# Performance work log

Hardware: AMD Instinct MI355X
Metric: run time of the kernel (lower is better)

Reference implementation:

```python
import jax, jax.numpy as jnp
import numpy as np

N = 100000   # nodes
E = 1600000  # edges
D = 64       # in_feats
H = 512      # hidden_dim
O = 64       # out_feats
K = 3        # hops
LN_EPS = 1e-5


def setup_inputs() -> dict:
    key = jax.random.key(0)
    ks = jax.random.split(key, 10)
    x = jax.random.normal(ks[0], (N, D), dtype=jnp.float32)
    edge_index = jax.random.randint(ks[1], (2, E), 0, N, dtype=jnp.int64)
    # SAGEConv lin_l weights (root_weight=False, bias=False): K stacked [D, D]
    w_prop = jax.random.normal(ks[2], (K, D, D), dtype=jnp.float32) / np.sqrt(D)
    lin1_w = jax.random.normal(ks[3], ((K + 1) * D, H), dtype=jnp.float32) / np.sqrt((K + 1) * D)
    lin1_b = jnp.zeros((H,), dtype=jnp.float32)
    ln_gamma = jnp.ones((H,), dtype=jnp.float32)
    ln_beta = jnp.zeros((H,), dtype=jnp.float32)
    lin2_w = jax.random.normal(ks[4], (H, O), dtype=jnp.float32) / np.sqrt(H)
    lin2_b = jnp.zeros((O,), dtype=jnp.float32)
    return {
        "x": x, "edge_index": edge_index, "w_prop": w_prop,
        "lin1_w": lin1_w, "lin1_b": lin1_b,
        "ln_gamma": ln_gamma, "ln_beta": ln_beta,
        "lin2_w": lin2_w, "lin2_b": lin2_b,
    }


def _sage_mean(h, src, dst, w):
    # mean-aggregate neighbor features at dst, then linear (no root, no bias)
    msg_sum = jax.ops.segment_sum(h[src], dst, num_segments=N)       # [N, D]
    deg = jax.ops.segment_sum(jnp.ones((E,), h.dtype), dst, num_segments=N)
    agg = msg_sum / jnp.maximum(deg, 1.0)[:, None]
    return agg @ w


def reference(x, edge_index, w_prop, lin1_w, lin1_b, ln_gamma, ln_beta, lin2_w, lin2_b):
    src, dst = edge_index[0], edge_index[1]
    zs = [x]
    curr = x
    for i in range(K):
        curr = _sage_mean(curr, src, dst, w_prop[i])
        zs.append(curr)
    h = jnp.concatenate(zs, axis=1)          # [N, (K+1)*D]
    h = h @ lin1_w + lin1_b                   # [N, H]
    mu = jnp.mean(h, axis=-1, keepdims=True)
    var = jnp.var(h, axis=-1, keepdims=True)
    h = (h - mu) * jax.lax.rsqrt(var + LN_EPS) * ln_gamma + ln_beta
    h = jax.nn.relu(h)
    # dropout is identity in eval mode (training=False)
    return h @ lin2_w + lin2_b                # [N, O]
```

## Files before the change

kernel.cpp:

```cpp
#include <hip/hip_runtime.h>

constexpr int NN = 100000;
constexpr int NE = 1600000;
constexpr int NBUK = 196;
constexpr int ECAP = 10240;
constexpr int CHUNK = 6250;
constexpr int NPT = 13;

typedef __attribute__((ext_vector_type(8))) short bf16x8;
typedef __attribute__((ext_vector_type(4))) float f32x4;

__device__ inline ushort f2b(float f){
  uint u = __float_as_uint(f);
  uint r = (u + 0x7FFFu + ((u >> 16) & 1u)) >> 16;
  return (ushort)r;
}
__device__ inline float b2f(ushort u){
  uint v = ((uint)u) << 16;
  return __uint_as_float(v);
}

template<int CTRL>
__device__ inline float dpp_xadd(float v){
  int j = __builtin_amdgcn_update_dpp(0, __float_as_int(v), CTRL, 0xF, 0xF, true);
  return v + __int_as_float(j);
}
__device__ inline float red16(float v){
  v = dpp_xadd<0xB1>(v);
  v = dpp_xadd<0x4E>(v);
  v = dpp_xadd<0x141>(v);
  v = dpp_xadd<0x140>(v);
  return v;
}

__global__ __launch_bounds__(512) void k_part1(const int* __restrict__ srcA,
                                               const int* __restrict__ dstA,
                                               int* __restrict__ bukcur,
                                               int* __restrict__ ebuf){
  __shared__ int stage[CHUNK];
  __shared__ unsigned char bstage[CHUNK];
  __shared__ int hist[256];
  __shared__ int lofs[256];
  __shared__ int lcur[NBUK];
  __shared__ int basebuf[NBUK];
  int t = threadIdx.x;
  int cbase = blockIdx.x * CHUNK;

  if (t < 256) hist[t] = 0;
  if (t < NBUK) lcur[t] = 0;
  __syncthreads();

  int pk[NPT], bb[NPT];
  #pragma unroll
  for (int j = 0; j < NPT; ++j){
    int i = t + j*512;
    bb[j] = -1;
    if (i < CHUNK){
      int e = cbase + i;
      int d = dstA[e];
      bb[j] = d >> 9;
      pk[j] = (srcA[e] << 9) | (d & 511);
      atomicAdd(&hist[bb[j]], 1);
    }
  }
  __syncthreads();

  int v = (t < 256) ? hist[t] : 0;
  if (t < 256) lofs[t] = v;
  __syncthreads();
  #pragma unroll
  for (int off = 1; off < 256; off <<= 1){
    int tv = (t < 256 && t >= off) ? lofs[t-off] : 0;
    __syncthreads();
    if (t < 256) lofs[t] += tv;
    __syncthreads();
  }
  if (t < 256) lofs[t] -= v;
  if (t < NBUK) basebuf[t] = atomicAdd(&bukcur[t], v);
  __syncthreads();

  #pragma unroll
  for (int j = 0; j < NPT; ++j){
    if (bb[j] >= 0){
      int p = atomicAdd(&lcur[bb[j]], 1);
      int slot = lofs[bb[j]] + p;
      stage[slot] = pk[j];
      bstage[slot] = (unsigned char)bb[j];
    }
  }
  __syncthreads();

  for (int i = t; i < CHUNK; i += 512){
    int b = bstage[i];
    int j = i - lofs[b];
    int pos = basebuf[b] + j;
    if (pos < ECAP) ebuf[b*ECAP + pos] = stage[i];
  }
}

__global__ void k_bscan(const int* __restrict__ bukcur, int* __restrict__ bukptr){
  __shared__ int s[256];
  int t = threadIdx.x;
  int v = (t < NBUK) ? bukcur[t] : 0;
  s[t] = v; __syncthreads();
  #pragma unroll
  for (int off = 1; off < 256; off <<= 1){
    int tv = (t >= off) ? s[t-off] : 0;
    __syncthreads();
    s[t] += tv;
    __syncthreads();
  }
  if (t < NBUK) bukptr[t] = s[t] - v;
  if (t == NBUK-1) bukptr[NBUK] = s[t];
}

__global__ __launch_bounds__(512) void k_bfinal(const int* __restrict__ ebuf,
                                                const int* __restrict__ bukcur,
                                                const int* __restrict__ bukptr,
                                                int* __restrict__ rowptr,
                                                int* __restrict__ csr){
  __shared__ int lcnt[512];
  __shared__ int lscan[512];
  __shared__ int lcur[512];
  int b = blockIdx.x, t = threadIdx.x;
  int cnt = bukcur[b]; if (cnt > ECAP) cnt = ECAP;
  int base = b*ECAP, gbase = bukptr[b];

  lcnt[t] = 0; lcur[t] = 0;
  __syncthreads();
  for (int i = t; i < cnt; i += 512) atomicAdd(&lcnt[ebuf[base+i] & 511], 1);
  __syncthreads();
  int v = lcnt[t];
  lscan[t] = v; __syncthreads();
  #pragma unroll
  for (int off = 1; off < 512; off <<= 1){
    int tv = (t >= off) ? lscan[t-off] : 0;
    __syncthreads();
    lscan[t] += tv;
    __syncthreads();
  }
  int excl = lscan[t] - v;
  lcnt[t] = excl;
  int node = b*512 + t;
  if (node <= NN) rowptr[node] = gbase + excl;
  __syncthreads();
  for (int i = t; i < cnt; i += 512){
    int p = ebuf[base+i];
    int d = p & 511;
    int pos = atomicAdd(&lcur[d], 1);
    csr[gbase + lcnt[d] + pos] = p >> 9;
  }
}

__global__ void k_xb(const float* __restrict__ x, ushort* __restrict__ xb){
  int i = blockIdx.x*256 + threadIdx.x;
  float4 v = ((const float4*)x)[i];
  ushort4 o;
  o.x = f2b(v.x); o.y = f2b(v.y); o.z = f2b(v.z); o.w = f2b(v.w);
  ((ushort4*)xb)[i] = o;
}

__global__ void k_vchain(const float* __restrict__ Wp, float* __restrict__ V2,
                         float* __restrict__ V3){
  __shared__ float sA[4096], sB[4096], sC[4096];
  int t = threadIdx.x;
  for (int i = t; i < 4096; i += 256){ sA[i] = Wp[i]; sB[i] = Wp[4096+i]; }
  __syncthreads();
  for (int i = t; i < 4096; i += 256){
    int r = i >> 6, c = i & 63; float s = 0.f;
    #pragma unroll 8
    for (int j = 0; j < 64; ++j) s += sA[r*64+j]*sB[j*64+c];
    sC[i] = s; V2[i] = s;
  }
  __syncthreads();
  for (int i = t; i < 4096; i += 256) sB[i] = Wp[8192+i];
  __syncthreads();
  for (int i = t; i < 4096; i += 256){
    int r = i >> 6, c = i & 63; float s = 0.f;
    #pragma unroll 8
    for (int j = 0; j < 64; ++j) s += sC[r*64+j]*sB[j*64+c];
    V3[i] = s;
  }
}

__global__ void k_ueff(const float* __restrict__ W1, const float* __restrict__ Wp,
                       const float* __restrict__ V2, const float* __restrict__ V3,
                       ushort* __restrict__ W1t){
  __shared__ float col[256];
  int c = blockIdx.x, r = threadIdx.x;
  col[r] = W1[(size_t)r*512 + c];
  __syncthreads();
  int p = r >> 6, i = r & 63;
  float s;
  if (p == 0) s = col[r];
  else {
    const float* V = (p == 1) ? Wp : (p == 2) ? V2 : V3;
    s = 0.f;
    #pragma unroll 8
    for (int j = 0; j < 64; ++j) s += V[i*64+j]*col[p*64+j];
  }
  W1t[c*256 + r] = f2b(s);
}

__global__ void k_w2t(const float* __restrict__ W2, ushort* __restrict__ W2t){
  int col = blockIdx.x, k = threadIdx.x;
  W2t[col*512 + k] = f2b(W2[(size_t)k*64 + col]);
}

__global__ void k_aggb(const ushort* __restrict__ hb, const int* __restrict__ rowptr,
                       const int* __restrict__ csr, ushort* __restrict__ yb){
  int lane = threadIdx.x & 63;
  int n = blockIdx.x*4 + (threadIdx.x >> 6);
  int f = lane & 7, s = lane >> 3;
  int beg = rowptr[n], end = rowptr[n+1];
  float a[8] = {};
  int e = beg + s;
  for (; e + 8 < end; e += 16){
    int i0 = csr[e], i1 = csr[e+8];
    bf16x8 v0 = *(const bf16x8*)(hb + (size_t)i0*64 + f*8);
    bf16x8 v1 = *(const bf16x8*)(hb + (size_t)i1*64 + f*8);
    #pragma unroll
    for (int j = 0; j < 8; ++j)
      a[j] += b2f((ushort)v0[j]) + b2f((ushort)v1[j]);
  }
  if (e < end){
    int i0 = csr[e];
    bf16x8 v = *(const bf16x8*)(hb + (size_t)i0*64 + f*8);
    #pragma unroll
    for (int j = 0; j < 8; ++j) a[j] += b2f((ushort)v[j]);
  }
  #pragma unroll
  for (int off = 8; off < 64; off <<= 1)
    #pragma unroll
    for (int j = 0; j < 8; ++j) a[j] += __shfl_xor(a[j], off);
  if (s == 0){
    float inv = 1.f / fmaxf((float)(end - beg), 1.f);
    bf16x8 o;
    #pragma unroll
    for (int j = 0; j < 8; ++j) o[j] = (short)f2b(a[j]*inv);
    *(bf16x8*)(yb + (size_t)n*64 + f*8) = o;
  }
}

__global__ __launch_bounds__(512, 4) void k_mlp(
    const ushort* __restrict__ cat0,
    const ushort* __restrict__ W1t, const float* __restrict__ b1,
    const float* __restrict__ gamma, const float* __restrict__ beta,
    const ushort* __restrict__ W2t, const float* __restrict__ b2,
    float* __restrict__ out){
  constexpr size_t PSTR = 6400000;
  __shared__ char lbuf[65536];
  __shared__ float2 s_pair[8][64];
  __shared__ float2 s_stat2[64];

  int tid = threadIdx.x;
  int lane = tid & 63, wv = tid >> 6;
  int l15 = lane & 15, l4 = lane >> 4;

  int bid = blockIdx.x;
  {
    constexpr int NB = 1563, q = NB/8, r = NB%8;
    int xcd = bid & 7, idx = bid >> 3;
    bid = (xcd < r ? xcd*(q+1) : r*(q+1) + (xcd-r)*q) + idx;
  }
  int nbase = bid * 64;

  #pragma unroll
  for (int i = 0; i < 4; ++i){
    int dest = (wv*4 + i)*1024 + lane*16;
    int row = dest >> 9;
    int kbyte = (dest & 511) ^ ((row & 7) << 4);
    const ushort* src = cat0 + (size_t)(kbyte >> 7)*PSTR
                             + (size_t)(nbase + row)*64 + ((kbyte & 127) >> 1);
    __builtin_amdgcn_global_load_lds(
        (const __attribute__((address_space(1))) void*)src,
        (__attribute__((address_space(3))) void*)(lbuf + (wv*4 + i)*1024),
        16, 0, 0);
  }
  __syncthreads();

  #define LOADA(kb, d)                                                          \
    { _Pragma("unroll")                                                         \
      for (int rt = 0; rt < 4; ++rt){                                           \
        int row_ = rt*16 + l15;                                                 \
        d[rt] = *(const bf16x8*)(lbuf + row_*512 +                              \
                 (((kb)*64 + l4*16) ^ ((row_ & 7) << 4)));                      \
      } }
  #define LOADB(kb, d)                                                          \
    { _Pragma("unroll")                                                         \
      for (int ci = 0; ci < 4; ++ci)                                            \
        d[ci] = *(const bf16x8*)(W1t + (size_t)(wv*64 + ci*16 + l15)*256 +      \
                                 (kb)*32 + l4*8); }

  f32x4 acc[4][4] = {};
  bf16x8 a[4], b[2][4];
  LOADB(0, b[0]);
  #pragma unroll
  for (int kb = 0; kb < 8; ++kb){
    int cur = kb & 1, nxt = cur ^ 1;
    if (kb < 7) LOADB(kb+1, b[nxt]);
    LOADA(kb, a);
    #pragma unroll
    for (int rt = 0; rt < 4; ++rt)
      #pragma unroll
      for (int ci = 0; ci < 4; ++ci)
        acc[rt][ci] = __builtin_amdgcn_mfma_f32_16x16x32_bf16(a[rt], b[cur][ci], acc[rt][ci], 0, 0, 0);
  }

  float bcol[4], gcol[4], ecol[4];
  #pragma unroll
  for (int ci = 0; ci < 4; ++ci){
    int col = wv*64 + ci*16 + l15;
    bcol[ci] = b1[col]; gcol[ci] = gamma[col]; ecol[ci] = beta[col];
  }
  #pragma unroll
  for (int rt = 0; rt < 4; ++rt)
    #pragma unroll
    for (int ci = 0; ci < 4; ++ci)
      #pragma unroll
      for (int r = 0; r < 4; ++r)
        acc[rt][ci][r] += bcol[ci];

  #pragma unroll
  for (int rt = 0; rt < 4; ++rt){
    #pragma unroll
    for (int r = 0; r < 4; ++r){
      float s = 0.f, q = 0.f;
      #pragma unroll
      for (int ci = 0; ci < 4; ++ci){
        float v = acc[rt][ci][r];
        s += v; q += v*v;
      }
      s = red16(s);
      q = red16(q);
      if (l15 == 0) s_pair[wv][rt*16 + l4*4 + r] = make_float2(s, q);
    }
  }
  __syncthreads();

  if (tid < 64){
    float s = 0.f, q = 0.f;
    #pragma unroll
    for (int w = 0; w < 8; ++w){ float2 p = s_pair[w][tid]; s += p.x; q += p.y; }
    float mu = s * (1.f/512.f);
    float var = q * (1.f/512.f) - mu*mu;
    s_stat2[tid] = make_float2(mu, rsqrtf(var + 1e-5f));
  }
  __syncthreads();

  #pragma unroll
  for (int rt = 0; rt < 4; ++rt){
    #pragma unroll
    for (int r = 0; r < 4; ++r){
      int row = rt*16 + l4*4 + r;
      float2 st = s_stat2[row];
      #pragma unroll
      for (int ci = 0; ci < 4; ++ci){
        float hv = fmaxf((acc[rt][ci][r] - st.x)*st.y*gcol[ci] + ecol[ci], 0.f);
        int col = wv*64 + ci*16 + l15;
        *((ushort*)(lbuf + row*1024 + ((col*2) ^ ((row & 7) << 4)))) = f2b(hv);
      }
    }
  }
  __syncthreads();

  #define LOADH(kb, d)                                                          \
    { _Pragma("unroll")                                                         \
      for (int t = 0; t < 2; ++t){                                              \
        int row_ = (rtb + t)*16 + l15;                                          \
        d[t] = *(const bf16x8*)(lbuf + row_*1024 +                              \
                 (((kb)*64 + l4*16) ^ ((row_ & 7) << 4)));                      \
      } }

  int ct = wv >> 1;
  int rtb = (wv & 1) * 2;
  f32x4 acc2[2] = {};
  const ushort* w2base = W2t + (size_t)(ct*16 + l15)*512 + l4*8;
  bf16x8 hb2[2][2], w2f[2];
  w2f[0] = *(const bf16x8*)(w2base);
  LOADH(0, hb2[0]);
  #pragma unroll
  for (int kb = 0; kb < 16; ++kb){
    int cur = kb & 1, nxt = cur ^ 1;
    if (kb < 15){
      w2f[nxt] = *(const bf16x8*)(w2base + (kb+1)*32);
      LOADH(kb+1, hb2[nxt]);
    }
    acc2[0] = __builtin_amdgcn_mfma_f32_16x16x32_bf16(hb2[cur][0], w2f[cur], acc2[0], 0, 0, 0);
    acc2[1] = __builtin_amdgcn_mfma_f32_16x16x32_bf16(hb2[cur][1], w2f[cur], acc2[1], 0, 0, 0);
  }

  float b2v = b2[ct*16 + l15];
  #pragma unroll
  for (int t = 0; t < 2; ++t){
    #pragma unroll
    for (int r = 0; r < 4; ++r){
      int row = (rtb + t)*16 + l4*4 + r;
      if (nbase + row < NN)
        out[(size_t)(nbase + row)*64 + ct*16 + l15] = acc2[t][r] + b2v;
    }
  }
  #undef LOADA
  #undef LOADB
  #undef LOADH
}

extern "C" void kernel_launch(void* const* d_in, const int* in_sizes, int n_in,
                              void* d_out, int out_size, void* d_ws, size_t ws_size,
                              hipStream_t stream){
  const float* x     = (const float*)d_in[0];
  const int*   eidx  = (const int*)d_in[1];
  const float* wprop = (const float*)d_in[2];
  const float* W1    = (const float*)d_in[3];
  const float* b1    = (const float*)d_in[4];
  const float* gamma = (const float*)d_in[5];
  const float* beta  = (const float*)d_in[6];
  const float* W2    = (const float*)d_in[7];
  const float* b2    = (const float*)d_in[8];
  float* out = (float*)d_out;
  const int* srcA = eidx;
  const int* dstA = eidx + NE;

  char* ws = (char*)d_ws;
  int*    rowptr = (int*)(ws);
  ushort* W1t    = (ushort*)(ws +   400384);
  ushort* W2t    = (ushort*)(ws +   662528);
  float*  V2     = (float*)(ws +    728064);
  float*  V3     = (float*)(ws +    744448);
  int*    bukcur = (int*)(ws +      760832);
  int*    bukptr = (int*)(ws +      761856);
  int*    csr    = (int*)(ws +      762880);
  int*    ebuf   = (int*)(ws +     7162880);
  ushort* xb     = (ushort*)(ws + 15191040);
  ushort* y1     = (ushort*)(ws + 27991040);
  ushort* y2     = (ushort*)(ws + 40791040);
  ushort* y3     = (ushort*)(ws + 53591040);

  hipMemsetAsync(bukcur, 0, NBUK*sizeof(int), stream);
  k_part1<<<256, 512, 0, stream>>>(srcA, dstA, bukcur, ebuf);
  k_bscan<<<1, 256, 0, stream>>>(bukcur, bukptr);
  k_bfinal<<<NBUK, 512, 0, stream>>>(ebuf, bukcur, bukptr, rowptr, csr);

  k_xb<<<6250, 256, 0, stream>>>(x, xb);
  k_vchain<<<1, 256, 0, stream>>>(wprop, V2, V3);
  k_ueff<<<512, 256, 0, stream>>>(W1, wprop, V2, V3, W1t);
  k_w2t<<<64, 512, 0, stream>>>(W2, W2t);

  k_aggb<<<25000, 256, 0, stream>>>(xb, rowptr, csr, y1);
  k_aggb<<<25000, 256, 0, stream>>>(y1, rowptr, csr, y2);
  k_aggb<<<25000, 256, 0, stream>>>(y2, rowptr, csr, y3);

  k_mlp<<<1563, 512, 0, stream>>>(xb, W1t, b1, gamma, beta, W2t, b2, out);
}
```

Measured before the change: 296.5 us.

## Assign one node per 8 lanes in aggregation, drop bucket scan, fuse bf16 cast

The CSR now uses fixed per-bucket bases (ECAP-strided) with separate begin and degree arrays, so the bucket prefix-scan kernel goes away. The x-to-bf16 conversion is folded into the partition kernel, removing another launch. Aggregation now gives each node an 8-lane group instead of a full wave, which removes the cross-lane shuffle reduction and uses all lanes on low-degree nodes. In exchange, each lane group walks its neighbour list serially, so load balance across high-degree nodes may suffer, and the padded CSR is sparser in memory.

```diff
diff --git a/kernel.cpp b/kernel.cpp
--- a/kernel.cpp
+++ b/kernel.cpp
@@ -36,7 +36,9 @@
 __global__ __launch_bounds__(512) void k_part1(const int* __restrict__ srcA,
                                                const int* __restrict__ dstA,
                                                int* __restrict__ bukcur,
-                                               int* __restrict__ ebuf){
+                                               int* __restrict__ ebuf,
+                                               const float* __restrict__ x,
+                                               ushort* __restrict__ xb){
   __shared__ int stage[CHUNK];
   __shared__ unsigned char bstage[CHUNK];
   __shared__ int hist[256];
@@ -96,35 +98,26 @@
     int pos = basebuf[b] + j;
     if (pos < ECAP) ebuf[b*ECAP + pos] = stage[i];
   }
-}
-
-__global__ void k_bscan(const int* __restrict__ bukcur, int* __restrict__ bukptr){
-  __shared__ int s[256];
-  int t = threadIdx.x;
-  int v = (t < NBUK) ? bukcur[t] : 0;
-  s[t] = v; __syncthreads();
-  #pragma unroll
-  for (int off = 1; off < 256; off <<= 1){
-    int tv = (t >= off) ? s[t-off] : 0;
-    __syncthreads();
-    s[t] += tv;
-    __syncthreads();
-  }
-  if (t < NBUK) bukptr[t] = s[t] - v;
-  if (t == NBUK-1) bukptr[NBUK] = s[t];
+
+  for (int i = blockIdx.x*512 + t; i < NN*16; i += 256*512){
+    float4 vv = ((const float4*)x)[i];
+    ushort4 o;
+    o.x = f2b(vv.x); o.y = f2b(vv.y); o.z = f2b(vv.z); o.w = f2b(vv.w);
+    ((ushort4*)xb)[i] = o;
+  }
 }
 
 __global__ __launch_bounds__(512) void k_bfinal(const int* __restrict__ ebuf,
                                                 const int* __restrict__ bukcur,
-                                                const int* __restrict__ bukptr,
-                                                int* __restrict__ rowptr,
+                                                int* __restrict__ rbeg,
+                                                int* __restrict__ degA,
                                                 int* __restrict__ csr){
   __shared__ int lcnt[512];
   __shared__ int lscan[512];
   __shared__ int lcur[512];
   int b = blockIdx.x, t = threadIdx.x;
   int cnt = bukcur[b]; if (cnt > ECAP) cnt = ECAP;
-  int base = b*ECAP, gbase = bukptr[b];
+  int base = b*ECAP, gbase = b*ECAP;
 
   lcnt[t] = 0; lcur[t] = 0;
   __syncthreads();
@@ -142,7 +135,7 @@
   int excl = lscan[t] - v;
   lcnt[t] = excl;
   int node = b*512 + t;
-  if (node <= NN) rowptr[node] = gbase + excl;
+  if (node < NN){ rbeg[node] = gbase + excl; degA[node] = v; }
   __syncthreads();
   for (int i = t; i < cnt; i += 512){
     int p = ebuf[base+i];
@@ -150,14 +143,6 @@
     int pos = atomicAdd(&lcur[d], 1);
     csr[gbase + lcnt[d] + pos] = p >> 9;
   }
-}
-
-__global__ void k_xb(const float* __restrict__ x, ushort* __restrict__ xb){
-  int i = blockIdx.x*256 + threadIdx.x;
-  float4 v = ((const float4*)x)[i];
-  ushort4 o;
-  o.x = f2b(v.x); o.y = f2b(v.y); o.z = f2b(v.z); o.w = f2b(v.w);
-  ((ushort4*)xb)[i] = o;
 }
 
 __global__ void k_vchain(const float* __restrict__ Wp, float* __restrict__ V2,
@@ -207,39 +192,35 @@
   W2t[col*512 + k] = f2b(W2[(size_t)k*64 + col]);
 }
 
-__global__ void k_aggb(const ushort* __restrict__ hb, const int* __restrict__ rowptr,
-                       const int* __restrict__ csr, ushort* __restrict__ yb){
+__global__ void k_aggb(const ushort* __restrict__ hb, const int* __restrict__ rbeg,
+                       const int* __restrict__ degA, const int* __restrict__ csr,
+                       ushort* __restrict__ yb){
   int lane = threadIdx.x & 63;
-  int n = blockIdx.x*4 + (threadIdx.x >> 6);
+  int wv = threadIdx.x >> 6;
   int f = lane & 7, s = lane >> 3;
-  int beg = rowptr[n], end = rowptr[n+1];
+  int n = blockIdx.x*32 + wv*8 + s;
+  int beg = rbeg[n], dg = degA[n];
   float a[8] = {};
-  int e = beg + s;
-  for (; e + 8 < end; e += 16){
-    int i0 = csr[e], i1 = csr[e+8];
+  int i = 0;
+  for (; i + 2 <= dg; i += 2){
+    int i0 = csr[beg+i], i1 = csr[beg+i+1];
     bf16x8 v0 = *(const bf16x8*)(hb + (size_t)i0*64 + f*8);
     bf16x8 v1 = *(const bf16x8*)(hb + (size_t)i1*64 + f*8);
     #pragma unroll
     for (int j = 0; j < 8; ++j)
       a[j] += b2f((ushort)v0[j]) + b2f((ushort)v1[j]);
   }
-  if (e < end){
-    int i0 = csr[e];
+  if (i < dg){
+    int i0 = csr[beg+i];
     bf16x8 v = *(const bf16x8*)(hb + (size_t)i0*64 + f*8);
     #pragma unroll
     for (int j = 0; j < 8; ++j) a[j] += b2f((ushort)v[j]);
   }
-  #pragma unroll
-  for (int off = 8; off < 64; off <<= 1)
-    #pragma unroll
-    for (int j = 0; j < 8; ++j) a[j] += __shfl_xor(a[j], off);
-  if (s == 0){
-    float inv = 1.f / fmaxf((float)(end - beg), 1.f);
-    bf16x8 o;
-    #pragma unroll
-    for (int j = 0; j < 8; ++j) o[j] = (short)f2b(a[j]*inv);
-    *(bf16x8*)(yb + (size_t)n*64 + f*8) = o;
-  }
+  float inv = 1.f / fmaxf((float)dg, 1.f);
+  bf16x8 o;
+  #pragma unroll
+  for (int j = 0; j < 8; ++j) o[j] = (short)f2b(a[j]*inv);
+  *(bf16x8*)(yb + (size_t)n*64 + f*8) = o;
 }
 
 __global__ __launch_bounds__(512, 4) void k_mlp(
@@ -422,33 +403,31 @@
   const int* dstA = eidx + NE;
 
   char* ws = (char*)d_ws;
-  int*    rowptr = (int*)(ws);
-  ushort* W1t    = (ushort*)(ws +   400384);
-  ushort* W2t    = (ushort*)(ws +   662528);
-  float*  V2     = (float*)(ws +    728064);
-  float*  V3     = (float*)(ws +    744448);
-  int*    bukcur = (int*)(ws +      760832);
-  int*    bukptr = (int*)(ws +      761856);
-  int*    csr    = (int*)(ws +      762880);
-  int*    ebuf   = (int*)(ws +     7162880);
-  ushort* xb     = (ushort*)(ws + 15191040);
-  ushort* y1     = (ushort*)(ws + 27991040);
-  ushort* y2     = (ushort*)(ws + 40791040);
-  ushort* y3     = (ushort*)(ws + 53591040);
+  int*    rbeg   = (int*)(ws);
+  int*    degA   = (int*)(ws +      400384);
+  ushort* W1t    = (ushort*)(ws +   800768);
+  ushort* W2t    = (ushort*)(ws +  1062912);
+  float*  V2     = (float*)(ws +   1128448);
+  float*  V3     = (float*)(ws +   1144832);
+  int*    bukcur = (int*)(ws +     1161216);
+  int*    csr    = (int*)(ws +     1162240);
+  int*    ebuf   = (int*)(ws +     9190400);
+  ushort* xb     = (ushort*)(ws + 17218560);
+  ushort* y1     = (ushort*)(ws + 30018560);
+  ushort* y2     = (ushort*)(ws + 42818560);
+  ushort* y3     = (ushort*)(ws + 55618560);
 
   hipMemsetAsync(bukcur, 0, NBUK*sizeof(int), stream);
-  k_part1<<<256, 512, 0, stream>>>(srcA, dstA, bukcur, ebuf);
-  k_bscan<<<1, 256, 0, stream>>>(bukcur, bukptr);
-  k_bfinal<<<NBUK, 512, 0, stream>>>(ebuf, bukcur, bukptr, rowptr, csr);
-
-  k_xb<<<6250, 256, 0, stream>>>(x, xb);
+  k_part1<<<256, 512, 0, stream>>>(srcA, dstA, bukcur, ebuf, x, xb);
+  k_bfinal<<<NBUK, 512, 0, stream>>>(ebuf, bukcur, rbeg, degA, csr);
+
   k_vchain<<<1, 256, 0, stream>>>(wprop, V2, V3);
   k_ueff<<<512, 256, 0, stream>>>(W1, wprop, V2, V3, W1t);
   k_w2t<<<64, 512, 0, stream>>>(W2, W2t);
 
-  k_aggb<<<25000, 256, 0, stream>>>(xb, rowptr, csr, y1);
-  k_aggb<<<25000, 256, 0, stream>>>(y1, rowptr, csr, y2);
-  k_aggb<<<25000, 256, 0, stream>>>(y2, rowptr, csr, y3);
+  k_aggb<<<3125, 256, 0, stream>>>(xb, rbeg, degA, csr, y1);
+  k_aggb<<<3125, 256, 0, stream>>>(y1, rbeg, degA, csr, y2);
+  k_aggb<<<3125, 256, 0, stream>>>(y2, rbeg, degA, csr, y3);
 
   k_mlp<<<1563, 512, 0, stream>>>(xb, W1t, b1, gamma, beta, W2t, b2, out);
 }
```

Result: faster. 271.2 us (-8.5%).
